# Kernel tuning notes

Hardware: AMD Instinct MI355X
Metric: run time of the kernel (lower is better)

Reference implementation:

```python
import jax, jax.numpy as jnp
import numpy as np

H = 256  # hidden_size == in_size
M = int(H * 4 / 3)  # 341, gated-MLP intermediate
EPS = 1e-5


def _layer_norm(x, w, b):
    mu = jnp.mean(x, axis=-1, keepdims=True)
    var = jnp.var(x, axis=-1, keepdims=True)
    return (x - mu) * jax.lax.rsqrt(var + EPS) * w + b


def setup_inputs() -> dict:
    key = jax.random.key(0)
    ks = jax.random.split(key, 8)
    s = 0.02
    inp = {
        "x": jax.random.normal(ks[0], (64, 2048, H), dtype=jnp.float32),
        "ln1_w": jnp.ones((H,), jnp.float32),
        "ln1_b": jnp.zeros((H,), jnp.float32),
        # sLSTM: stacked [z, i, f, o] input and recurrent weights
        "W": jax.random.normal(ks[1], (4 * H, H), jnp.float32) * s,
        "R": jax.random.normal(ks[2], (4 * H, H), jnp.float32) * s,
        "b": jnp.zeros((4 * H,), jnp.float32),
        "up_W": jax.random.normal(ks[3], (M, H), jnp.float32) * s,
        "up_b": jnp.zeros((M,), jnp.float32),
        "gate_W": jax.random.normal(ks[4], (M, H), jnp.float32) * s,
        "gate_b": jnp.zeros((M,), jnp.float32),
        "down_W": jax.random.normal(ks[5], (H, M), jnp.float32) * s,
        "down_b": jnp.zeros((H,), jnp.float32),
        "ln2_w": jnp.ones((H,), jnp.float32),
        "ln2_b": jnp.zeros((H,), jnp.float32),
    }
    return inp


def _slstm(nx, W, R, b):
    # nx: (B, T, H) -> all hidden states (B, T, H)
    B, T, _ = nx.shape
    xW = jnp.einsum("bth,gh->btg", nx, W) + b  # (B, T, 4H)
    xW = jnp.swapaxes(xW, 0, 1)  # (T, B, 4H)

    def step(carry, xw_t):
        h, c, n, m = carry  # each (B, H)
        pre = xw_t + h @ R.T
        z = jnp.tanh(pre[:, :H])
        log_i = pre[:, H:2 * H]
        log_f = pre[:, 2 * H:3 * H]
        o = jax.nn.sigmoid(pre[:, 3 * H:])
        m_new = jnp.maximum(log_f + m, log_i)  # stabilizer
        i_g = jnp.exp(log_i - m_new)
        f_g = jnp.exp(log_f + m - m_new)
        c = f_g * c + i_g * z
        n = f_g * n + i_g
        h = o * (c / n)
        return (h, c, n, m_new), h

    z0 = jnp.zeros((B, H), nx.dtype)
    (_, _, _, _), hs = jax.lax.scan(step, (z0, z0, z0, z0), xW)
    return jnp.swapaxes(hs, 0, 1)  # (B, T, H)


def reference(x, ln1_w, ln1_b, W, R, b, up_W, up_b, gate_W, gate_b,
              down_W, down_b, ln2_w, ln2_b):
    residual = x
    nx = _layer_norm(x, ln1_w, ln1_b)
    lstm_out = _slstm(nx, W, R, b)
    gate_signal = jax.nn.gelu(jnp.einsum("bth,mh->btm", lstm_out, gate_W) + gate_b)
    mlp_inter = jnp.einsum("bth,mh->btm", lstm_out, up_W) + up_b
    mlp_out = jnp.einsum("btm,hm->bth", gate_signal * mlp_inter, down_W) + down_b
    return _layer_norm(mlp_out, ln2_w, ln2_b) + residual
```

## Files before the change

kernel.cpp:

```cpp
#include <hip/hip_runtime.h>
#include <hip/hip_bf16.h>
#include <hip/hip_fp16.h>

typedef _Float16 f16;
typedef __hip_bfloat16 bf16;
typedef short bf16x8 __attribute__((ext_vector_type(8)));
typedef float f32x4 __attribute__((ext_vector_type(4)));
typedef _Float16 f16x2 __attribute__((ext_vector_type(2)));

#define HDIM 256
#define G4   1024
#define TT   2048
#define NB   64
#define NTOK (64*2048)
#define MPAD 384

__device__ __forceinline__ int dot4i(unsigned a, unsigned b, int c) {
#if __has_builtin(__builtin_amdgcn_sdot4)
    return __builtin_amdgcn_sdot4((int)a, (int)b, c, false);
#else
    char4 x = __builtin_bit_cast(char4, a), y = __builtin_bit_cast(char4, b);
    return c + (int)x.x*(int)y.x + (int)x.y*(int)y.y + (int)x.z*(int)y.z + (int)x.w*(int)y.w;
#endif
}

__device__ __forceinline__ int quad_red(int v) {
#if __has_builtin(__builtin_amdgcn_update_dpp)
    v += __builtin_amdgcn_update_dpp(0, v, 0xB1, 0xF, 0xF, true);
    v += __builtin_amdgcn_update_dpp(0, v, 0x4E, 0xF, 0xF, true);
    return v;
#else
    v += __shfl_xor(v, 1, 64);
    v += __shfl_xor(v, 2, 64);
    return v;
#endif
}

__device__ __forceinline__ float gelu_tanh(float x) {
    float x3 = x*x*x;
    float t = tanhf(0.7978845608028654f * (x + 0.044715f * x3));
    return 0.5f * x * (1.0f + t);
}

__global__ void k_prep_w(const float* __restrict__ W, bf16* __restrict__ Wb) {
    int i = blockIdx.x*256 + threadIdx.x;
    Wb[i] = __float2bfloat16(W[i]);
}

__global__ __launch_bounds__(256) void k_prep_r8(const float* __restrict__ R,
        char* __restrict__ R8, float* __restrict__ rscale) {
    int wave = threadIdx.x >> 6, lane = threadIdx.x & 63;
    int g = blockIdx.x*4 + wave;
    float4 v = ((const float4*)(R + (long)g*256))[lane];
    float mx = fmaxf(fmaxf(fabsf(v.x), fabsf(v.y)), fmaxf(fabsf(v.z), fabsf(v.w)));
    #pragma unroll
    for (int m = 1; m < 64; m <<= 1) mx = fmaxf(mx, __shfl_xor(mx, m, 64));
    float inv = (mx > 0.f) ? 127.f/mx : 0.f;
    int q0 = (int)rintf(v.x*inv), q1 = (int)rintf(v.y*inv);
    int q2 = (int)rintf(v.z*inv), q3 = (int)rintf(v.w*inv);
    unsigned packed = (q0 & 0xff) | ((q1 & 0xff) << 8) | ((q2 & 0xff) << 16) | ((q3 & 0xff) << 24);
    ((unsigned*)(R8 + (long)g*256))[lane] = packed;
    if (lane == 0) rscale[g] = mx * (1.0f/127.f);
}

__global__ void k_prep_gu(const float* __restrict__ gW, const float* __restrict__ uW,
                          const float* __restrict__ gb, const float* __restrict__ ub,
                          bf16* __restrict__ gWb, bf16* __restrict__ uWb,
                          float* __restrict__ gbp, float* __restrict__ ubp) {
    int i = blockIdx.x*256 + threadIdx.x;
    int r = i >> 8, c = i & 255;
    gWb[i] = __float2bfloat16(r < 341 ? gW[r*256 + c] : 0.f);
    uWb[i] = __float2bfloat16(r < 341 ? uW[r*256 + c] : 0.f);
    if (i < 384) {
        gbp[i] = i < 341 ? gb[i] : 0.f;
        ubp[i] = i < 341 ? ub[i] : 0.f;
    }
}

__global__ void k_prep_down(const float* __restrict__ dW, bf16* __restrict__ dWb) {
    int i = blockIdx.x*256 + threadIdx.x;
    int r = i / 384, c = i % 384;
    dWb[i] = __float2bfloat16(c < 341 ? dW[r*341 + c] : 0.f);
}

__global__ __launch_bounds__(256) void k_ln1(const float* __restrict__ x,
        const float* __restrict__ w, const float* __restrict__ b,
        bf16* __restrict__ nx) {
    int wave = threadIdx.x >> 6, lane = threadIdx.x & 63;
    long tok = (long)blockIdx.x * 4 + wave;
    float4 v = ((const float4*)(x + tok*HDIM))[lane];
    float s = v.x + v.y + v.z + v.w;
    float q = v.x*v.x + v.y*v.y + v.z*v.z + v.w*v.w;
    #pragma unroll
    for (int m = 1; m < 64; m <<= 1) { s += __shfl_xor(s, m, 64); q += __shfl_xor(q, m, 64); }
    float mean = s * (1.0f/HDIM);
    float rs = rsqrtf(q*(1.0f/HDIM) - mean*mean + 1e-5f);
    float4 wv = ((const float4*)w)[lane];
    float4 bv = ((const float4*)b)[lane];
    bf16 tmp[4];
    tmp[0] = __float2bfloat16((v.x-mean)*rs*wv.x + bv.x);
    tmp[1] = __float2bfloat16((v.y-mean)*rs*wv.y + bv.y);
    tmp[2] = __float2bfloat16((v.z-mean)*rs*wv.z + bv.z);
    tmp[3] = __float2bfloat16((v.w-mean)*rs*wv.w + bv.w);
    *(ushort4*)(nx + tok*HDIM + lane*4) = *(ushort4*)tmp;
}

__global__ __launch_bounds__(256) void k_ln2(const f16* __restrict__ mlp,
        const float* __restrict__ x, const float* __restrict__ w,
        const float* __restrict__ b, float* __restrict__ out) {
    int wave = threadIdx.x >> 6, lane = threadIdx.x & 63;
    long tok = (long)blockIdx.x * 4 + wave;
    const f16* mr = mlp + tok*HDIM + lane*4;
    float4 v; v.x = (float)mr[0]; v.y = (float)mr[1]; v.z = (float)mr[2]; v.w = (float)mr[3];
    float s = v.x + v.y + v.z + v.w;
    float q = v.x*v.x + v.y*v.y + v.z*v.z + v.w*v.w;
    #pragma unroll
    for (int m = 1; m < 64; m <<= 1) { s += __shfl_xor(s, m, 64); q += __shfl_xor(q, m, 64); }
    float mean = s * (1.0f/HDIM);
    float rs = rsqrtf(q*(1.0f/HDIM) - mean*mean + 1e-5f);
    float4 wv = ((const float4*)w)[lane];
    float4 bv = ((const float4*)b)[lane];
    float4 xv = ((const float4*)(x + tok*HDIM))[lane];
    float4 ov;
    ov.x = (v.x-mean)*rs*wv.x + bv.x + xv.x;
    ov.y = (v.y-mean)*rs*wv.y + bv.y + xv.y;
    ov.z = (v.z-mean)*rs*wv.z + bv.z + xv.z;
    ov.w = (v.w-mean)*rs*wv.w + bv.w + xv.w;
    ((float4*)(out + tok*HDIM))[lane] = ov;
}

enum { MODE_F16 = 0, MODE_GELU_F16 = 1, MODE_MUL_BF16 = 2, MODE_XW_F16 = 3 };

template<int MODE>
__global__ __launch_bounds__(256) void k_gemm(
    const bf16* __restrict__ A, const bf16* __restrict__ Bm,
    const float* __restrict__ bias, void* __restrict__ Cv,
    const f16* __restrict__ gatebuf,
    int K, int lda, int ldb, int ldc, int ldg)
{
    __shared__ char Al[128*128];
    __shared__ char Bl[64*128];
    const int tid = threadIdx.x;
    const long bm = (long)blockIdx.x * 128;
    const int bn = blockIdx.y * 64;
    const int wave = tid >> 6, lane = tid & 63;
    const int wm = wave >> 1, wn = wave & 1;
    const int l16 = lane & 15, lq = lane >> 4;
    f32x4 acc[4][2] = {};
    for (int k0 = 0; k0 < K; k0 += 64) {
        #pragma unroll
        for (int p = 0; p < 4; ++p) {
            int ci = tid + p*256;
            int row = ci >> 3, s = ci & 7;
            uint4 d = *(const uint4*)(A + (bm + row)*lda + k0 + s*8);
            *(uint4*)(Al + row*128 + ((s ^ (row&7))<<4)) = d;
        }
        #pragma unroll
        for (int p = 0; p < 2; ++p) {
            int ci = tid + p*256;
            int row = ci >> 3, s = ci & 7;
            uint4 d = *(const uint4*)(Bm + (long)(bn + row)*ldb + k0 + s*8);
            *(uint4*)(Bl + row*128 + ((s ^ (row&7))<<4)) = d;
        }
        __syncthreads();
        #pragma unroll
        for (int kc = 0; kc < 2; ++kc) {
            bf16x8 bf[2];
            #pragma unroll
            for (int fn = 0; fn < 2; ++fn) {
                int row = wn*32 + fn*16 + l16;
                int slot = (kc<<2) + lq;
                bf[fn] = *(const bf16x8*)(Bl + row*128 + ((slot ^ (row&7))<<4));
            }
            #pragma unroll
            for (int fm = 0; fm < 4; ++fm) {
                int row = wm*64 + fm*16 + l16;
                int slot = (kc<<2) + lq;
                bf16x8 af = *(const bf16x8*)(Al + row*128 + ((slot ^ (row&7))<<4));
                acc[fm][0] = __builtin_amdgcn_mfma_f32_16x16x32_bf16(af, bf[0], acc[fm][0], 0,0,0);
                acc[fm][1] = __builtin_amdgcn_mfma_f32_16x16x32_bf16(af, bf[1], acc[fm][1], 0,0,0);
            }
        }
        __syncthreads();
    }
    #pragma unroll
    for (int fm = 0; fm < 4; ++fm) {
        #pragma unroll
        for (int fn = 0; fn < 2; ++fn) {
            int n = bn + wn*32 + fn*16 + l16;
            float bv = bias[n];
            #pragma unroll
            for (int r = 0; r < 4; ++r) {
                long m = bm + wm*64 + fm*16 + lq*4 + r;
                float v = acc[fm][fn][r] + bv;
                if constexpr (MODE == MODE_F16) {
                    ((f16*)Cv)[m*ldc + n] = (f16)v;
                } else if constexpr (MODE == MODE_XW_F16) {
                    ((f16*)Cv)[m*ldc + ((n & 255) << 2) + (n >> 8)] = (f16)v;
                } else if constexpr (MODE == MODE_GELU_F16) {
                    ((f16*)Cv)[m*ldc + n] = (f16)gelu_tanh(v);
                } else {
                    float g = (float)gatebuf[m*ldg + n];
                    ((bf16*)Cv)[m*ldc + n] = __float2bfloat16(g * v);
                }
            }
        }
    }
}


#define SCAN_STEP(XREG, TPRE)                                                   \
    do {                                                                        \
        f16x2 xlo = __builtin_bit_cast(f16x2, XREG.x);                          \
        f16x2 xhi = __builtin_bit_cast(f16x2, XREG.y);                          \
        XREG = *(const uint2*)(xg + (long)(TPRE)*2048);                         \
        const uint4* hh4 = (const uint4*)(hq[cur] + kg*64);                     \
        int S0 = 0, S1 = 0, S2 = 0, S3 = 0;                                     \
        _Pragma("unroll")                                                       \
        for (int c = 0; c < 4; ++c) {                                           \
            uint4 hh = hh4[c];                                                  \
            uint4 r0 = Rr[0][c], r1 = Rr[1][c], r2 = Rr[2][c], r3 = Rr[3][c];   \
            S0 = dot4i(r0.x, hh.x, S0); S0 = dot4i(r0.y, hh.y, S0);             \
            S0 = dot4i(r0.z, hh.z, S0); S0 = dot4i(r0.w, hh.w, S0);             \
            S1 = dot4i(r1.x, hh.x, S1); S1 = dot4i(r1.y, hh.y, S1);             \
            S1 = dot4i(r1.z, hh.z, S1); S1 = dot4i(r1.w, hh.w, S1);             \
            S2 = dot4i(r2.x, hh.x, S2); S2 = dot4i(r2.y, hh.y, S2);             \
            S2 = dot4i(r2.z, hh.z, S2); S2 = dot4i(r2.w, hh.w, S2);             \
            S3 = dot4i(r3.x, hh.x, S3); S3 = dot4i(r3.y, hh.y, S3);             \
            S3 = dot4i(r3.z, hh.z, S3); S3 = dot4i(r3.w, hh.w, S3);             \
        }                                                                       \
        S0 = quad_red(S0); S1 = quad_red(S1);                                   \
        S2 = quad_red(S2); S3 = quad_red(S3);                                   \
        float pz = rs[0]*(float)S0 + (float)xlo[0];                             \
        float pi = rs[1]*(float)S1 + (float)xlo[1];                             \
        float pf = rs[2]*(float)S2 + (float)xhi[0];                             \
        float po = rs[3]*(float)S3 + (float)xhi[1];                             \
        float e = __expf(-2.0f * fabsf(pz));                                    \
        float z = copysignf((1.0f - e) / (1.0f + e), pz);                       \
        float o = 1.0f / (1.0f + __expf(-po));                                  \
        float mn = fmaxf(pf + mst, pi);                                         \
        float ig = __expf(pi - mn);                                             \
        float fg = __expf(pf + mst - mn);                                       \
        cst = fg*cst + ig*z;                                                    \
        nst = fg*nst + ig;                                                      \
        mst = mn;                                                               \
        float h = o * (cst / nst);                                              \
        if (kg == 0) {                                                          \
            hq[cur^1][gb] = (char)(int)rintf(h * 127.f);                        \
            hrow[gb] = __float2bfloat16(h);                                     \
        }                                                                       \
        __builtin_amdgcn_sched_barrier(0);                                      \
        asm volatile("s_waitcnt lgkmcnt(0)" ::: "memory");                      \
        __builtin_amdgcn_s_barrier();                                           \
        __builtin_amdgcn_sched_barrier(0);                                      \
        cur ^= 1;                                                               \
        hrow += HDIM;                                                           \
    } while (0)

__global__ __launch_bounds__(1024) __attribute__((amdgpu_waves_per_eu(4, 4)))
void k_scan(const f16* __restrict__ xW, const char* __restrict__ R8,
            const float* __restrict__ rscale, bf16* __restrict__ h_out)
{
    __shared__ char hq[2][256];
    const int tid = threadIdx.x;
    const int b   = blockIdx.x;
    const int kg  = tid & 3;
    const int gb  = tid >> 2;

    uint4 Rr[4][4];
    float rs[4];
    #pragma unroll
    for (int m = 0; m < 4; ++m) {
        const uint4* rp = (const uint4*)(R8 + (long)(gb + 256*m)*256 + kg*64);
        #pragma unroll
        for (int c = 0; c < 4; ++c) Rr[m][c] = rp[c];
        rs[m] = rscale[gb + 256*m] * (1.0f/127.0f);
    }
    if (tid < 64) ((unsigned*)hq[0])[tid] = 0u;

    const char* xg = (const char*)xW + (long)b * TT * 2048 + gb*8;
    bf16* hrow = h_out + (long)b * TT * HDIM;

    uint2 XA = *(const uint2*)(xg);
    uint2 XB = *(const uint2*)(xg + 2048);
    float cst = 0.f, nst = 0.f, mst = 0.f;
    int cur = 0;
    __syncthreads();

    for (int t = 0; t < TT; t += 2) {
        SCAN_STEP(XA, t + 2);
        SCAN_STEP(XB, t + 3);
    }
}

extern "C" void kernel_launch(void* const* d_in, const int* in_sizes, int n_in,
                              void* d_out, int out_size, void* d_ws, size_t ws_size,
                              hipStream_t stream) {
    const float* x     = (const float*)d_in[0];
    const float* ln1w  = (const float*)d_in[1];
    const float* ln1b  = (const float*)d_in[2];
    const float* W     = (const float*)d_in[3];
    const float* R     = (const float*)d_in[4];
    const float* bg    = (const float*)d_in[5];
    const float* upW   = (const float*)d_in[6];
    const float* upb   = (const float*)d_in[7];
    const float* gateW = (const float*)d_in[8];
    const float* gateb = (const float*)d_in[9];
    const float* downW = (const float*)d_in[10];
    const float* downb = (const float*)d_in[11];
    const float* ln2w  = (const float*)d_in[12];
    const float* ln2b  = (const float*)d_in[13];

    char* ws = (char*)d_ws;
    size_t off = 0;
    auto alloc = [&](size_t bytes) { char* p = ws + off; off += (bytes + 255) & ~255ULL; return p; };
    f16*  mlp16   = (f16*)alloc((size_t)NTOK*HDIM*2);
    char* regionB = alloc((size_t)NTOK*G4*2);
    bf16* h       = (bf16*)alloc((size_t)NTOK*HDIM*2);
    bf16* Wb      = (bf16*)alloc(262144*2);
    char* R8      = (char*)alloc(262144);
    float* rscale = (float*)alloc(1024*4);
    bf16* gWb     = (bf16*)alloc((size_t)MPAD*256*2);
    bf16* uWb     = (bf16*)alloc((size_t)MPAD*256*2);
    bf16* dWb     = (bf16*)alloc((size_t)256*MPAD*2);
    float* gbp    = (float*)alloc(MPAD*4);
    float* ubp    = (float*)alloc(MPAD*4);

    bf16* nx       = (bf16*)mlp16;
    f16*  xWb      = (f16*)regionB;
    f16*  gate_out = (f16*)regionB;
    bf16* prod     = (bf16*)(regionB + (size_t)NTOK*MPAD*2);

    k_prep_w   <<<1024, 256, 0, stream>>>(W, Wb);
    k_prep_r8  <<<256, 256, 0, stream>>>(R, R8, rscale);
    k_prep_gu  <<<384, 256, 0, stream>>>(gateW, upW, gateb, upb, gWb, uWb, gbp, ubp);
    k_prep_down<<<384, 256, 0, stream>>>(downW, dWb);
    k_ln1      <<<NTOK/4, 256, 0, stream>>>(x, ln1w, ln1b, nx);
    k_gemm<MODE_XW_F16><<<dim3(1024, 16), 256, 0, stream>>>(nx, Wb, bg, xWb, nullptr, 256, 256, 256, 1024, 0);
    k_scan     <<<64, 1024, 0, stream>>>(xWb, R8, rscale, h);
    k_gemm<MODE_GELU_F16><<<dim3(1024, 6), 256, 0, stream>>>(h, gWb, gbp, gate_out, nullptr, 256, 256, 256, MPAD, 0);
    k_gemm<MODE_MUL_BF16><<<dim3(1024, 6), 256, 0, stream>>>(h, uWb, ubp, prod, gate_out, 256, 256, 256, MPAD, MPAD);
    k_gemm<MODE_F16><<<dim3(1024, 4), 256, 0, stream>>>(prod, dWb, downb, mlp16, nullptr, MPAD, MPAD, MPAD, HDIM, 0);
    k_ln2      <<<NTOK/4, 256, 0, stream>>>(mlp16, x, ln2w, ln2b, (float*)d_out);
}
```

Before: 3.065 ms.

## Compute sLSTM recurrent matvec with int8 MFMA instead of sdot4 lanes

The recurrent h·R^T product in the scan moves from per-lane sdot4 chains with DPP quad reductions to int8 MFMA 16x16x64 instructions. The hidden vector is broadcast as the A operand and R slices sit in registers as B fragments. The block shrinks from 1024 to 512 threads, each lane now owns two hidden units, and only row 0 of each MFMA output is used. This aims to shorten the per-timestep latency on the serial critical path, but wastes 15/16 of the MFMA work and relies on the MFMA result layout being correct.

```diff
diff --git a/kernel.cpp b/kernel.cpp
--- a/kernel.cpp
+++ b/kernel.cpp
@@ -6,6 +6,7 @@
 typedef __hip_bfloat16 bf16;
 typedef short bf16x8 __attribute__((ext_vector_type(8)));
 typedef float f32x4 __attribute__((ext_vector_type(4)));
+typedef int i32x4 __attribute__((ext_vector_type(4)));
 typedef _Float16 f16x2 __attribute__((ext_vector_type(2)));
 
 #define HDIM 256
@@ -14,27 +15,6 @@
 #define NB   64
 #define NTOK (64*2048)
 #define MPAD 384
-
-__device__ __forceinline__ int dot4i(unsigned a, unsigned b, int c) {
-#if __has_builtin(__builtin_amdgcn_sdot4)
-    return __builtin_amdgcn_sdot4((int)a, (int)b, c, false);
-#else
-    char4 x = __builtin_bit_cast(char4, a), y = __builtin_bit_cast(char4, b);
-    return c + (int)x.x*(int)y.x + (int)x.y*(int)y.y + (int)x.z*(int)y.z + (int)x.w*(int)y.w;
-#endif
-}
-
-__device__ __forceinline__ int quad_red(int v) {
-#if __has_builtin(__builtin_amdgcn_update_dpp)
-    v += __builtin_amdgcn_update_dpp(0, v, 0xB1, 0xF, 0xF, true);
-    v += __builtin_amdgcn_update_dpp(0, v, 0x4E, 0xF, 0xF, true);
-    return v;
-#else
-    v += __shfl_xor(v, 1, 64);
-    v += __shfl_xor(v, 2, 64);
-    return v;
-#endif
-}
 
 __device__ __forceinline__ float gelu_tanh(float x) {
     float x3 = x*x*x;
@@ -209,45 +189,105 @@
 }
 
 
-#define SCAN_STEP(XREG, TPRE)                                                   \
+__global__ __launch_bounds__(512) __attribute__((amdgpu_waves_per_eu(2, 2)))
+void k_scan(const f16* __restrict__ xW, const char* __restrict__ R8,
+            const float* __restrict__ rscale, bf16* __restrict__ h_out)
+{
+    __shared__ char hq[2][256];
+    const int tid = threadIdx.x;
+    const int b    = blockIdx.x;
+    const int w    = tid >> 6;
+    const int lane = tid & 63;
+    const int c    = lane & 15;
+    const int q    = lane >> 4;
+    const int j0   = w*32 + c;
+    const int j1   = j0 + 16;
+
+    uint4 Bf0[4][4], Bf1[4][4];
+    #pragma unroll
+    for (int m = 0; m < 4; ++m) {
+        #pragma unroll
+        for (int kk = 0; kk < 4; ++kk) {
+            Bf0[m][kk] = *(const uint4*)(R8 + (long)(j0 + 256*m)*256 + kk*64 + q*16);
+            Bf1[m][kk] = *(const uint4*)(R8 + (long)(j1 + 256*m)*256 + kk*64 + q*16);
+        }
+    }
+    float rs0[4], rs1[4];
+    #pragma unroll
+    for (int m = 0; m < 4; ++m) {
+        rs0[m] = rscale[j0 + 256*m] * (1.0f/127.0f);
+        rs1[m] = rscale[j1 + 256*m] * (1.0f/127.0f);
+    }
+    if (tid < 64) ((unsigned*)hq[0])[tid] = 0u;
+
+    const char* xg = (const char*)xW + (long)b * TT * 2048;
+    bf16* hrow = h_out + (long)b * TT * HDIM;
+
+    uint2 XA0 = *(const uint2*)(xg + j0*8);
+    uint2 XA1 = *(const uint2*)(xg + j1*8);
+    uint2 XB0 = *(const uint2*)(xg + 2048 + j0*8);
+    uint2 XB1 = *(const uint2*)(xg + 2048 + j1*8);
+    float cst0 = 0.f, nst0 = 0.f, mst0 = 0.f;
+    float cst1 = 0.f, nst1 = 0.f, mst1 = 0.f;
+    int cur = 0;
+    __syncthreads();
+
+#define SLSTM_EPI(PZ, PI, PF, PO, CST, NST, MST, HOUT)                          \
     do {                                                                        \
-        f16x2 xlo = __builtin_bit_cast(f16x2, XREG.x);                          \
-        f16x2 xhi = __builtin_bit_cast(f16x2, XREG.y);                          \
-        XREG = *(const uint2*)(xg + (long)(TPRE)*2048);                         \
-        const uint4* hh4 = (const uint4*)(hq[cur] + kg*64);                     \
-        int S0 = 0, S1 = 0, S2 = 0, S3 = 0;                                     \
+        float e = __expf(-2.0f * fabsf(PZ));                                    \
+        float z = copysignf((1.0f - e) / (1.0f + e), PZ);                       \
+        float o = 1.0f / (1.0f + __expf(-(PO)));                                \
+        float mn = fmaxf((PF) + MST, PI);                                       \
+        float ig = __expf((PI) - mn);                                           \
+        float fg = __expf((PF) + MST - mn);                                     \
+        CST = fg*CST + ig*z;                                                    \
+        NST = fg*NST + ig;                                                      \
+        MST = mn;                                                               \
+        HOUT = o * (CST / NST);                                                 \
+    } while (0)
+
+#define SCAN_STEP(X0, X1, TPRE)                                                 \
+    do {                                                                        \
+        f16x2 x0lo = __builtin_bit_cast(f16x2, X0.x);                           \
+        f16x2 x0hi = __builtin_bit_cast(f16x2, X0.y);                           \
+        f16x2 x1lo = __builtin_bit_cast(f16x2, X1.x);                           \
+        f16x2 x1hi = __builtin_bit_cast(f16x2, X1.y);                           \
+        X0 = *(const uint2*)(xg + (long)(TPRE)*2048 + j0*8);                    \
+        X1 = *(const uint2*)(xg + (long)(TPRE)*2048 + j1*8);                    \
+        i32x4 af[4];                                                            \
         _Pragma("unroll")                                                       \
-        for (int c = 0; c < 4; ++c) {                                           \
-            uint4 hh = hh4[c];                                                  \
-            uint4 r0 = Rr[0][c], r1 = Rr[1][c], r2 = Rr[2][c], r3 = Rr[3][c];   \
-            S0 = dot4i(r0.x, hh.x, S0); S0 = dot4i(r0.y, hh.y, S0);             \
-            S0 = dot4i(r0.z, hh.z, S0); S0 = dot4i(r0.w, hh.w, S0);             \
-            S1 = dot4i(r1.x, hh.x, S1); S1 = dot4i(r1.y, hh.y, S1);             \
-            S1 = dot4i(r1.z, hh.z, S1); S1 = dot4i(r1.w, hh.w, S1);             \
-            S2 = dot4i(r2.x, hh.x, S2); S2 = dot4i(r2.y, hh.y, S2);             \
-            S2 = dot4i(r2.z, hh.z, S2); S2 = dot4i(r2.w, hh.w, S2);             \
-            S3 = dot4i(r3.x, hh.x, S3); S3 = dot4i(r3.y, hh.y, S3);             \
-            S3 = dot4i(r3.z, hh.z, S3); S3 = dot4i(r3.w, hh.w, S3);             \
+        for (int kk = 0; kk < 4; ++kk)                                          \
+            af[kk] = __builtin_bit_cast(i32x4,                                  \
+                         *(const uint4*)(hq[cur] + kk*64 + q*16));              \
+        i32x4 ac00 = {0,0,0,0}, ac01 = {0,0,0,0}, ac02 = {0,0,0,0}, ac03 = {0,0,0,0}; \
+        i32x4 ac10 = {0,0,0,0}, ac11 = {0,0,0,0}, ac12 = {0,0,0,0}, ac13 = {0,0,0,0}; \
+        _Pragma("unroll")                                                       \
+        for (int kk = 0; kk < 4; ++kk) {                                        \
+            ac00 = __builtin_amdgcn_mfma_i32_16x16x64_i8(af[kk], __builtin_bit_cast(i32x4, Bf0[0][kk]), ac00, 0,0,0); \
+            ac01 = __builtin_amdgcn_mfma_i32_16x16x64_i8(af[kk], __builtin_bit_cast(i32x4, Bf0[1][kk]), ac01, 0,0,0); \
+            ac02 = __builtin_amdgcn_mfma_i32_16x16x64_i8(af[kk], __builtin_bit_cast(i32x4, Bf0[2][kk]), ac02, 0,0,0); \
+            ac03 = __builtin_amdgcn_mfma_i32_16x16x64_i8(af[kk], __builtin_bit_cast(i32x4, Bf0[3][kk]), ac03, 0,0,0); \
+            ac10 = __builtin_amdgcn_mfma_i32_16x16x64_i8(af[kk], __builtin_bit_cast(i32x4, Bf1[0][kk]), ac10, 0,0,0); \
+            ac11 = __builtin_amdgcn_mfma_i32_16x16x64_i8(af[kk], __builtin_bit_cast(i32x4, Bf1[1][kk]), ac11, 0,0,0); \
+            ac12 = __builtin_amdgcn_mfma_i32_16x16x64_i8(af[kk], __builtin_bit_cast(i32x4, Bf1[2][kk]), ac12, 0,0,0); \
+            ac13 = __builtin_amdgcn_mfma_i32_16x16x64_i8(af[kk], __builtin_bit_cast(i32x4, Bf1[3][kk]), ac13, 0,0,0); \
         }                                                                       \
-        S0 = quad_red(S0); S1 = quad_red(S1);                                   \
-        S2 = quad_red(S2); S3 = quad_red(S3);                                   \
-        float pz = rs[0]*(float)S0 + (float)xlo[0];                             \
-        float pi = rs[1]*(float)S1 + (float)xlo[1];                             \
-        float pf = rs[2]*(float)S2 + (float)xhi[0];                             \
-        float po = rs[3]*(float)S3 + (float)xhi[1];                             \
-        float e = __expf(-2.0f * fabsf(pz));                                    \
-        float z = copysignf((1.0f - e) / (1.0f + e), pz);                       \
-        float o = 1.0f / (1.0f + __expf(-po));                                  \
-        float mn = fmaxf(pf + mst, pi);                                         \
-        float ig = __expf(pi - mn);                                             \
-        float fg = __expf(pf + mst - mn);                                       \
-        cst = fg*cst + ig*z;                                                    \
-        nst = fg*nst + ig;                                                      \
-        mst = mn;                                                               \
-        float h = o * (cst / nst);                                              \
-        if (kg == 0) {                                                          \
-            hq[cur^1][gb] = (char)(int)rintf(h * 127.f);                        \
-            hrow[gb] = __float2bfloat16(h);                                     \
+        float pz0 = rs0[0]*(float)ac00[0] + (float)x0lo[0];                     \
+        float pi0 = rs0[1]*(float)ac01[0] + (float)x0lo[1];                     \
+        float pf0 = rs0[2]*(float)ac02[0] + (float)x0hi[0];                     \
+        float po0 = rs0[3]*(float)ac03[0] + (float)x0hi[1];                     \
+        float pz1 = rs1[0]*(float)ac10[0] + (float)x1lo[0];                     \
+        float pi1 = rs1[1]*(float)ac11[0] + (float)x1lo[1];                     \
+        float pf1 = rs1[2]*(float)ac12[0] + (float)x1hi[0];                     \
+        float po1 = rs1[3]*(float)ac13[0] + (float)x1hi[1];                     \
+        float h0, h1;                                                           \
+        SLSTM_EPI(pz0, pi0, pf0, po0, cst0, nst0, mst0, h0);                    \
+        SLSTM_EPI(pz1, pi1, pf1, po1, cst1, nst1, mst1, h1);                    \
+        if (q == 0) {                                                           \
+            hq[cur^1][j0] = (char)(int)rintf(h0 * 127.f);                       \
+            hq[cur^1][j1] = (char)(int)rintf(h1 * 127.f);                       \
+            hrow[j0] = __float2bfloat16(h0);                                    \
+            hrow[j1] = __float2bfloat16(h1);                                    \
         }                                                                       \
         __builtin_amdgcn_sched_barrier(0);                                      \
         asm volatile("s_waitcnt lgkmcnt(0)" ::: "memory");                      \
@@ -257,40 +297,12 @@
         hrow += HDIM;                                                           \
     } while (0)
 
-__global__ __launch_bounds__(1024) __attribute__((amdgpu_waves_per_eu(4, 4)))
-void k_scan(const f16* __restrict__ xW, const char* __restrict__ R8,
-            const float* __restrict__ rscale, bf16* __restrict__ h_out)
-{
-    __shared__ char hq[2][256];
-    const int tid = threadIdx.x;
-    const int b   = blockIdx.x;
-    const int kg  = tid & 3;
-    const int gb  = tid >> 2;
-
-    uint4 Rr[4][4];
-    float rs[4];
-    #pragma unroll
-    for (int m = 0; m < 4; ++m) {
-        const uint4* rp = (const uint4*)(R8 + (long)(gb + 256*m)*256 + kg*64);
-        #pragma unroll
-        for (int c = 0; c < 4; ++c) Rr[m][c] = rp[c];
-        rs[m] = rscale[gb + 256*m] * (1.0f/127.0f);
-    }
-    if (tid < 64) ((unsigned*)hq[0])[tid] = 0u;
-
-    const char* xg = (const char*)xW + (long)b * TT * 2048 + gb*8;
-    bf16* hrow = h_out + (long)b * TT * HDIM;
-
-    uint2 XA = *(const uint2*)(xg);
-    uint2 XB = *(const uint2*)(xg + 2048);
-    float cst = 0.f, nst = 0.f, mst = 0.f;
-    int cur = 0;
-    __syncthreads();
-
     for (int t = 0; t < TT; t += 2) {
-        SCAN_STEP(XA, t + 2);
-        SCAN_STEP(XB, t + 3);
-    }
+        SCAN_STEP(XA0, XA1, t + 2);
+        SCAN_STEP(XB0, XB1, t + 3);
+    }
+#undef SCAN_STEP
+#undef SLSTM_EPI
 }
 
 extern "C" void kernel_launch(void* const* d_in, const int* in_sizes, int n_in,
@@ -337,7 +349,7 @@
     k_prep_down<<<384, 256, 0, stream>>>(downW, dWb);
     k_ln1      <<<NTOK/4, 256, 0, stream>>>(x, ln1w, ln1b, nx);
     k_gemm<MODE_XW_F16><<<dim3(1024, 16), 256, 0, stream>>>(nx, Wb, bg, xWb, nullptr, 256, 256, 256, 1024, 0);
-    k_scan     <<<64, 1024, 0, stream>>>(xWb, R8, rscale, h);
+    k_scan     <<<64, 512, 0, stream>>>(xWb, R8, rscale, h);
     k_gemm<MODE_GELU_F16><<<dim3(1024, 6), 256, 0, stream>>>(h, gWb, gbp, gate_out, nullptr, 256, 256, 256, MPAD, 0);
     k_gemm<MODE_MUL_BF16><<<dim3(1024, 6), 256, 0, stream>>>(h, uWb, ubp, prod, gate_out, 256, 256, 256, MPAD, MPAD);
     k_gemm<MODE_F16><<<dim3(1024, 4), 256, 0, stream>>>(prod, dWb, downb, mlp16, nullptr, MPAD, MPAD, MPAD, HDIM, 0);
```

New measurement: 2.739 ms. 1.12x faster.

## Compute sLSTM recurrent matvec with int8 MFMA instead of sdot4 plus DPP reduction

Applied to the files above, without the earlier changes.

The per-timestep recurrent product h·R^T in the scan kernel now uses mfma_i32_16x16x64_i8. The quantized h vector is broadcast as the A operand to all rows, and R stays resident in registers as B fragments. This replaces 64 sdot4 instructions and a quad DPP reduction per thread with 16 MFMA ops per wave, aiming to shorten the serial step latency. Only row 0 of each accumulator is used, so 15/16 of the MFMA work is wasted, and MFMA latency may dominate at this small size.

```diff
diff --git a/kernel.cpp b/kernel.cpp
--- a/kernel.cpp
+++ b/kernel.cpp
@@ -6,6 +6,7 @@
 typedef __hip_bfloat16 bf16;
 typedef short bf16x8 __attribute__((ext_vector_type(8)));
 typedef float f32x4 __attribute__((ext_vector_type(4)));
+typedef int i32x4 __attribute__((ext_vector_type(4)));
 typedef _Float16 f16x2 __attribute__((ext_vector_type(2)));
 
 #define HDIM 256
@@ -14,27 +15,6 @@
 #define NB   64
 #define NTOK (64*2048)
 #define MPAD 384
-
-__device__ __forceinline__ int dot4i(unsigned a, unsigned b, int c) {
-#if __has_builtin(__builtin_amdgcn_sdot4)
-    return __builtin_amdgcn_sdot4((int)a, (int)b, c, false);
-#else
-    char4 x = __builtin_bit_cast(char4, a), y = __builtin_bit_cast(char4, b);
-    return c + (int)x.x*(int)y.x + (int)x.y*(int)y.y + (int)x.z*(int)y.z + (int)x.w*(int)y.w;
-#endif
-}
-
-__device__ __forceinline__ int quad_red(int v) {
-#if __has_builtin(__builtin_amdgcn_update_dpp)
-    v += __builtin_amdgcn_update_dpp(0, v, 0xB1, 0xF, 0xF, true);
-    v += __builtin_amdgcn_update_dpp(0, v, 0x4E, 0xF, 0xF, true);
-    return v;
-#else
-    v += __shfl_xor(v, 1, 64);
-    v += __shfl_xor(v, 2, 64);
-    return v;
-#endif
-}
 
 __device__ __forceinline__ float gelu_tanh(float x) {
     float x3 = x*x*x;
@@ -209,32 +189,63 @@
 }
 
 
+__global__ __launch_bounds__(1024) __attribute__((amdgpu_waves_per_eu(4, 4)))
+void k_scan(const f16* __restrict__ xW, const char* __restrict__ R8,
+            const float* __restrict__ rscale, bf16* __restrict__ h_out)
+{
+    __shared__ char hq[2][256];
+    const int tid = threadIdx.x;
+    const int b    = blockIdx.x;
+    const int w    = tid >> 6;
+    const int lane = tid & 63;
+    const int c    = lane & 15;
+    const int q    = lane >> 4;
+    const int j    = w*16 + c;
+
+    uint4 Bf[4][4];
+    #pragma unroll
+    for (int m = 0; m < 4; ++m) {
+        #pragma unroll
+        for (int kk = 0; kk < 4; ++kk)
+            Bf[m][kk] = *(const uint4*)(R8 + (long)(j + 256*m)*256 + kk*64 + q*16);
+    }
+    float rs[4];
+    #pragma unroll
+    for (int m = 0; m < 4; ++m)
+        rs[m] = rscale[j + 256*m] * (1.0f/127.0f);
+    if (tid < 64) ((unsigned*)hq[0])[tid] = 0u;
+
+    const char* xg = (const char*)xW + (long)b * TT * 2048 + j*8;
+    bf16* hrow = h_out + (long)b * TT * HDIM;
+
+    uint2 XA = *(const uint2*)(xg);
+    uint2 XB = *(const uint2*)(xg + 2048);
+    float cst = 0.f, nst = 0.f, mst = 0.f;
+    int cur = 0;
+    __syncthreads();
+
 #define SCAN_STEP(XREG, TPRE)                                                   \
     do {                                                                        \
         f16x2 xlo = __builtin_bit_cast(f16x2, XREG.x);                          \
         f16x2 xhi = __builtin_bit_cast(f16x2, XREG.y);                          \
         XREG = *(const uint2*)(xg + (long)(TPRE)*2048);                         \
-        const uint4* hh4 = (const uint4*)(hq[cur] + kg*64);                     \
-        int S0 = 0, S1 = 0, S2 = 0, S3 = 0;                                     \
+        i32x4 af[4];                                                            \
         _Pragma("unroll")                                                       \
-        for (int c = 0; c < 4; ++c) {                                           \
-            uint4 hh = hh4[c];                                                  \
-            uint4 r0 = Rr[0][c], r1 = Rr[1][c], r2 = Rr[2][c], r3 = Rr[3][c];   \
-            S0 = dot4i(r0.x, hh.x, S0); S0 = dot4i(r0.y, hh.y, S0);             \
-            S0 = dot4i(r0.z, hh.z, S0); S0 = dot4i(r0.w, hh.w, S0);             \
-            S1 = dot4i(r1.x, hh.x, S1); S1 = dot4i(r1.y, hh.y, S1);             \
-            S1 = dot4i(r1.z, hh.z, S1); S1 = dot4i(r1.w, hh.w, S1);             \
-            S2 = dot4i(r2.x, hh.x, S2); S2 = dot4i(r2.y, hh.y, S2);             \
-            S2 = dot4i(r2.z, hh.z, S2); S2 = dot4i(r2.w, hh.w, S2);             \
-            S3 = dot4i(r3.x, hh.x, S3); S3 = dot4i(r3.y, hh.y, S3);             \
-            S3 = dot4i(r3.z, hh.z, S3); S3 = dot4i(r3.w, hh.w, S3);             \
+        for (int kk = 0; kk < 4; ++kk)                                          \
+            af[kk] = __builtin_bit_cast(i32x4,                                  \
+                         *(const uint4*)(hq[cur] + kk*64 + q*16));              \
+        i32x4 ac0 = {0,0,0,0}, ac1 = {0,0,0,0}, ac2 = {0,0,0,0}, ac3 = {0,0,0,0}; \
+        _Pragma("unroll")                                                       \
+        for (int kk = 0; kk < 4; ++kk) {                                        \
+            ac0 = __builtin_amdgcn_mfma_i32_16x16x64_i8(af[kk], __builtin_bit_cast(i32x4, Bf[0][kk]), ac0, 0,0,0); \
+            ac1 = __builtin_amdgcn_mfma_i32_16x16x64_i8(af[kk], __builtin_bit_cast(i32x4, Bf[1][kk]), ac1, 0,0,0); \
+            ac2 = __builtin_amdgcn_mfma_i32_16x16x64_i8(af[kk], __builtin_bit_cast(i32x4, Bf[2][kk]), ac2, 0,0,0); \
+            ac3 = __builtin_amdgcn_mfma_i32_16x16x64_i8(af[kk], __builtin_bit_cast(i32x4, Bf[3][kk]), ac3, 0,0,0); \
         }                                                                       \
-        S0 = quad_red(S0); S1 = quad_red(S1);                                   \
-        S2 = quad_red(S2); S3 = quad_red(S3);                                   \
-        float pz = rs[0]*(float)S0 + (float)xlo[0];                             \
-        float pi = rs[1]*(float)S1 + (float)xlo[1];                             \
-        float pf = rs[2]*(float)S2 + (float)xhi[0];                             \
-        float po = rs[3]*(float)S3 + (float)xhi[1];                             \
+        float pz = rs[0]*(float)ac0[0] + (float)xlo[0];                         \
+        float pi = rs[1]*(float)ac1[0] + (float)xlo[1];                         \
+        float pf = rs[2]*(float)ac2[0] + (float)xhi[0];                         \
+        float po = rs[3]*(float)ac3[0] + (float)xhi[1];                         \
         float e = __expf(-2.0f * fabsf(pz));                                    \
         float z = copysignf((1.0f - e) / (1.0f + e), pz);                       \
         float o = 1.0f / (1.0f + __expf(-po));                                  \
@@ -245,9 +256,9 @@
         nst = fg*nst + ig;                                                      \
         mst = mn;                                                               \
         float h = o * (cst / nst);                                              \
-        if (kg == 0) {                                                          \
-            hq[cur^1][gb] = (char)(int)rintf(h * 127.f);                        \
-            hrow[gb] = __float2bfloat16(h);                                     \
+        if (q == 0) {                                                           \
+            hq[cur^1][j] = (char)(int)rintf(h * 127.f);                         \
+            hrow[j] = __float2bfloat16(h);                                      \
         }                                                                       \
         __builtin_amdgcn_sched_barrier(0);                                      \
         asm volatile("s_waitcnt lgkmcnt(0)" ::: "memory");                      \
@@ -257,40 +268,11 @@
         hrow += HDIM;                                                           \
     } while (0)
 
-__global__ __launch_bounds__(1024) __attribute__((amdgpu_waves_per_eu(4, 4)))
-void k_scan(const f16* __restrict__ xW, const char* __restrict__ R8,
-            const float* __restrict__ rscale, bf16* __restrict__ h_out)
-{
-    __shared__ char hq[2][256];
-    const int tid = threadIdx.x;
-    const int b   = blockIdx.x;
-    const int kg  = tid & 3;
-    const int gb  = tid >> 2;
-
-    uint4 Rr[4][4];
-    float rs[4];
-    #pragma unroll
-    for (int m = 0; m < 4; ++m) {
-        const uint4* rp = (const uint4*)(R8 + (long)(gb + 256*m)*256 + kg*64);
-        #pragma unroll
-        for (int c = 0; c < 4; ++c) Rr[m][c] = rp[c];
-        rs[m] = rscale[gb + 256*m] * (1.0f/127.0f);
-    }
-    if (tid < 64) ((unsigned*)hq[0])[tid] = 0u;
-
-    const char* xg = (const char*)xW + (long)b * TT * 2048 + gb*8;
-    bf16* hrow = h_out + (long)b * TT * HDIM;
-
-    uint2 XA = *(const uint2*)(xg);
-    uint2 XB = *(const uint2*)(xg + 2048);
-    float cst = 0.f, nst = 0.f, mst = 0.f;
-    int cur = 0;
-    __syncthreads();
-
     for (int t = 0; t < TT; t += 2) {
         SCAN_STEP(XA, t + 2);
         SCAN_STEP(XB, t + 3);
     }
+#undef SCAN_STEP
 }
 
 extern "C" void kernel_launch(void* const* d_in, const int* in_sizes, int n_in,
```

New measurement: 2.566 ms, median of 2. 1.19x faster.
